# Kernel optimization log

Hardware: AMD Instinct MI355X
Metric: run time of the kernel (lower is better)

Reference implementation:

```python
import jax, jax.numpy as jnp
import numpy as np

NPOINT = 1024   # samples (farthest point sampling count)
RADIUS = 0.2    # ball query radius
K = 32          # neighbors per ball


def farthest_point_sample(xyz, npoint):
    # xyz: [B, N, 3] -> idx: [B, npoint] int32
    B, N, _ = xyz.shape
    def body(carry, _):
        dists, farthest = carry                      # [B,N], [B]
        centroid = jnp.take_along_axis(xyz, farthest[:, None, None], axis=1)  # [B,1,3]
        d = jnp.sum((xyz - centroid) ** 2, axis=-1)  # [B,N]
        dists = jnp.minimum(dists, d)
        nxt = jnp.argmax(dists, axis=-1).astype(jnp.int32)
        return (dists, nxt), farthest
    init = (jnp.full((B, N), 1e10, dtype=xyz.dtype), jnp.zeros((B,), jnp.int32))
    _, idx = jax.lax.scan(body, init, None, length=npoint)
    return jnp.transpose(idx)  # [B, npoint]


def query_ball_point(radius, k, xyz, new_xyz):
    # returns idx: [B, S, k] int32 -- first k in-radius point indices,
    # padded with the first found index (TF query_ball_point semantics)
    N = xyz.shape[1]
    sqd = jnp.sum((new_xyz[:, :, None, :] - xyz[:, None, :, :]) ** 2, axis=-1)  # [B,S,N]
    cand = jnp.where(sqd <= radius * radius, jnp.arange(N, dtype=jnp.int32)[None, None, :], N)
    idx = jnp.sort(cand, axis=-1)[..., :k]          # [B,S,k]
    first = idx[..., :1]
    return jnp.where(idx == N, first, idx).astype(jnp.int32)


def group_point(x, idx):
    # x: [B,N,C], idx: [B,S,k] -> [B,S,k,C]
    return jax.vmap(lambda xb, ib: xb[ib])(x, idx)


def setup_inputs() -> dict:
    key = jax.random.key(0)
    ks = jax.random.split(key, 8)
    B, N, C = 16, 4096, 64
    xyz = jax.random.uniform(ks[0], (B, N, 3), dtype=jnp.float32)
    points = jax.random.normal(ks[1], (B, N, C), dtype=jnp.float32)
    cin = 3 + C  # use_xyz concat
    widths = [64, 64, 128]
    W, b, c = [], [], cin
    for i, w in enumerate(widths):
        W.append(jax.random.normal(ks[2 + i], (c, w), dtype=jnp.float32) * (1.0 / np.sqrt(c)))
        b.append(jnp.zeros((w,), dtype=jnp.float32))
        c = w
    return {"xyz": xyz, "points": points,
            "W0": W[0], "b0": b[0], "W1": W[1], "b1": b[1], "W2": W[2], "b2": b[2]}


def reference(xyz, points, W0, b0, W1, b1, W2, b2):
    # --- sample_and_group ---
    fps_idx = farthest_point_sample(xyz, NPOINT)                 # [B,S]
    new_xyz = jax.vmap(lambda xb, ib: xb[ib])(xyz, fps_idx)      # [B,S,3]
    idx = query_ball_point(RADIUS, K, xyz, new_xyz)              # [B,S,K]
    grouped_xyz = group_point(xyz, idx) - new_xyz[:, :, None, :] # [B,S,K,3]
    grouped_points = group_point(points, idx)                    # [B,S,K,C]
    new_points = jnp.concatenate([grouped_xyz, grouped_points], axis=-1)  # [B,S,K,3+C]
    # --- shared 1x1-conv MLP (bn=False, relu) ---
    for W, bb in ((W0, b0), (W1, b1), (W2, b2)):
        new_points = jax.nn.relu(jnp.einsum('bskc,cd->bskd', new_points, W) + bb)
    # --- max pool over neighborhood ---
    new_points = jnp.max(new_points, axis=2)                     # [B,S,Cout]
    return new_xyz, new_points, idx
```

## Files before the change

### kernel.cpp

```cpp
#include <hip/hip_runtime.h>

#define BB 16
#define NN 4096
#define SS 1024
#define KNB 32
#define FPT 16
#define FNW 4

typedef unsigned long long ull;

__device__ __forceinline__ float sqd3(float dx, float dy, float dz) {
    return __fadd_rn(__fadd_rn(__fmul_rn(dx, dx), __fmul_rn(dy, dy)), __fmul_rn(dz, dz));
}

#define DPPMAX(m, ctrl, rm)                                                              \
    {                                                                                    \
        unsigned _t = (unsigned)__builtin_amdgcn_update_dpp((int)(m), (int)(m), (ctrl),  \
                                                            (rm), 0xf, false);           \
        (m) = ((m) > _t) ? (m) : _t;                                                     \
    }

__global__ __launch_bounds__(256) void fused1_kernel(const float* __restrict__ xyz,
                                                     const float* __restrict__ points,
                                                     const float* __restrict__ W0,
                                                     const float* __restrict__ b0,
                                                     float* __restrict__ P1,
                                                     float* __restrict__ out_newxyz) {
    __shared__ union {
        struct {
            float4 pts[NN];
            ull    keys[2][FNW];
            int    hist[SS];
        } f;
        float w0s[67 * 64];
    } sm;

    const int t = threadIdx.x;

    if (blockIdx.x < BB) {
        const int b = blockIdx.x;
        const int lane = t & 63;
        const float* src = xyz + (size_t)b * (NN * 3) + (size_t)t * (FPT * 3);

        float px[FPT], py[FPT], pz[FPT], dist[FPT];
        {
            float c48[48];
#pragma unroll
            for (int m = 0; m < 12; ++m) {
                float4 v = ((const float4*)src)[m];
                c48[4 * m + 0] = v.x; c48[4 * m + 1] = v.y;
                c48[4 * m + 2] = v.z; c48[4 * m + 3] = v.w;
            }
#pragma unroll
            for (int j = 0; j < FPT; ++j) {
                px[j] = c48[3 * j + 0];
                py[j] = c48[3 * j + 1];
                pz[j] = c48[3 * j + 2];
                dist[j] = 1e10f;
                sm.f.pts[t * FPT + j] = make_float4(px[j], py[j], pz[j], 0.f);
            }
        }
        __syncthreads();

        int far = 0;
        for (int it = 0; it < SS; ++it) {
            if (t == 0) sm.f.hist[it] = far;
            if (it == SS - 1) break;
            float4 c = sm.f.pts[far];

            float bv = -1.f;
            int bn = 0;
#pragma unroll
            for (int j = 0; j < FPT; ++j) {
                float d = sqd3(px[j] - c.x, py[j] - c.y, pz[j] - c.z);
                float dj = fminf(dist[j], d);
                dist[j] = dj;
                bool g = dj > bv;
                bv = g ? dj : bv;
                bn = g ? (t * FPT + j) : bn;
            }

            unsigned mb = __float_as_uint(bv);
            DPPMAX(mb, 0x111, 0xf);
            DPPMAX(mb, 0x112, 0xf);
            DPPMAX(mb, 0x114, 0xf);
            DPPMAX(mb, 0x118, 0xf);
            DPPMAX(mb, 0x142, 0xa);
            DPPMAX(mb, 0x143, 0xc);
            unsigned vmb = (unsigned)__builtin_amdgcn_readlane((int)mb, 63);

            ull ball = __ballot(__float_as_uint(bv) == vmb);
            int sel = __ffsll(ball) - 1;
            int widx = __builtin_amdgcn_readlane(bn, sel);

            const int par = it & 1;
            if (lane == 0) {
                const int wv = t >> 6;
                sm.f.keys[par][wv] = ((ull)vmb << 32) | (unsigned)(~widx);
            }
            __syncthreads();
            const ull* kp = &sm.f.keys[par][0];
            ull k0 = kp[0], k1 = kp[1], k2 = kp[2], k3 = kp[3];
            ull a0 = (k0 > k1) ? k0 : k1;
            ull a1 = (k2 > k3) ? k2 : k3;
            ull best = (a0 > a1) ? a0 : a1;
            far = (int)(~(unsigned)best);
        }
        __syncthreads();
#pragma unroll
        for (int r = 0; r < 4; ++r) {
            int it2 = t + 256 * r;
            int fi = sm.f.hist[it2];
            float4 c = sm.f.pts[fi];
            size_t o = ((size_t)b * SS + it2) * 3;
            out_newxyz[o + 0] = c.x;
            out_newxyz[o + 1] = c.y;
            out_newxyz[o + 2] = c.z;
        }
    } else {
        for (int i = t; i < 67 * 64; i += 256) sm.w0s[i] = W0[i];
        __syncthreads();
        const int lane = t & 63;
        const int wv = t >> 6;
        const float bias = b0[lane];
        const int base = (blockIdx.x - BB) * 256 + wv * 64;
        for (int pi = 0; pi < 64; ++pi) {
            const int n = base + pi;
            const float* xp = xyz + (size_t)n * 3;
            const float* pp = points + (size_t)n * 64;
            float acc = bias;
            acc = fmaf(xp[0], sm.w0s[0 * 64 + lane], acc);
            acc = fmaf(xp[1], sm.w0s[1 * 64 + lane], acc);
            acc = fmaf(xp[2], sm.w0s[2 * 64 + lane], acc);
#pragma unroll 8
            for (int c = 0; c < 64; ++c) acc = fmaf(pp[c], sm.w0s[(3 + c) * 64 + lane], acc);
            P1[(size_t)n * 64 + lane] = acc;
        }
    }
}

__global__ __launch_bounds__(256) void k3_kernel(const float* __restrict__ xyz,
                                                 const float* __restrict__ P1,
                                                 const float* __restrict__ W0,
                                                 const float* __restrict__ W1,
                                                 const float* __restrict__ b1,
                                                 const float* __restrict__ W2,
                                                 const float* __restrict__ b2,
                                                 float* __restrict__ d_out) {
    const int t = threadIdx.x;
    const int lane = t & 63;
    const int wv = t >> 6;
    const int b = blockIdx.x >> 10;

    __shared__ int   ids[KNB];
    __shared__ int   s_cnt;
    __shared__ float part[4][128];
    __shared__ float h1s[4][8][64];
    __shared__ float h2s[4][8][64];

    float* out_newxyz = d_out;
    float* out_points = d_out + (size_t)BB * SS * 3;
    float* out_idx    = d_out + (size_t)BB * SS * 3 + (size_t)BB * SS * 128;

    const size_t q = (size_t)blockIdx.x;
    const float nx = out_newxyz[q * 3 + 0];
    const float ny = out_newxyz[q * 3 + 1];
    const float nz = out_newxyz[q * 3 + 2];

    if (wv == 0) {
        const float* xb = xyz + (size_t)b * (NN * 3);
        const float R2 = 0.04f;
        const ull ltmask = (1ull << lane) - 1ull;
        int total = 0;
        for (int c0 = 0; c0 < NN && total < KNB; c0 += 128) {
            const float* xp0 = xb + (size_t)(c0 + lane) * 3;
            const float* xp1 = xb + (size_t)(c0 + 64 + lane) * 3;
            float d0 = sqd3(xp0[0] - nx, xp0[1] - ny, xp0[2] - nz);
            float d1 = sqd3(xp1[0] - nx, xp1[1] - ny, xp1[2] - nz);
            bool in0 = (d0 <= R2);
            bool in1 = (d1 <= R2);
            ull m0 = __ballot(in0);
            ull m1 = __ballot(in1);
            int pc0 = __popcll(m0);
            int pos0 = total + __popcll(m0 & ltmask);
            int pos1 = total + pc0 + __popcll(m1 & ltmask);
            if (in0 && pos0 < KNB) ids[pos0] = c0 + lane;
            if (in1 && pos1 < KNB) ids[pos1] = c0 + 64 + lane;
            total += pc0 + __popcll(m1);
        }
        if (lane == 0) s_cnt = (total < KNB) ? total : KNB;
    }

    const float qv = nx * W0[lane] + ny * W0[64 + lane] + nz * W0[128 + lane];

    float w1col[64];
#pragma unroll
    for (int i = 0; i < 64; ++i) w1col[i] = W1[i * 64 + lane];
    const float b1v = b1[lane];

    __syncthreads();
    const int cnt = s_cnt;
    if (t >= cnt && t < KNB) ids[t] = ids[0];
    __syncthreads();
    if (t < KNB) out_idx[q * KNB + t] = (float)ids[t];

    const float* P1b = P1 + (size_t)b * NN * 64;
#pragma unroll
    for (int kk = 0; kk < 8; ++kk) {
        int n = ids[wv * 8 + kk];
        float v = P1b[(size_t)n * 64 + lane] - qv;
        h1s[wv][kk][lane] = fmaxf(v, 0.f);
    }

    float acc[8];
#pragma unroll
    for (int kk = 0; kk < 8; ++kk) acc[kk] = b1v;
#pragma unroll
    for (int qd = 0; qd < 16; ++qd) {
#pragma unroll
        for (int kk = 0; kk < 8; ++kk) {
            float4 h4 = *(const float4*)&h1s[wv][kk][4 * qd];
            acc[kk] = fmaf(h4.x, w1col[4 * qd + 0], acc[kk]);
            acc[kk] = fmaf(h4.y, w1col[4 * qd + 1], acc[kk]);
            acc[kk] = fmaf(h4.z, w1col[4 * qd + 2], acc[kk]);
            acc[kk] = fmaf(h4.w, w1col[4 * qd + 3], acc[kk]);
        }
    }
#pragma unroll
    for (int kk = 0; kk < 8; ++kk) h2s[wv][kk][lane] = fmaxf(acc[kk], 0.f);

    float outmax[2];
#pragma unroll
    for (int p = 0; p < 2; ++p) {
        float w2col[64];
#pragma unroll
        for (int i = 0; i < 64; ++i) w2col[i] = W2[i * 128 + 64 * p + lane];
        const float b2v = b2[64 * p + lane];
        float acc3[8];
#pragma unroll
        for (int kk = 0; kk < 8; ++kk) acc3[kk] = b2v;
#pragma unroll
        for (int qd = 0; qd < 16; ++qd) {
#pragma unroll
            for (int kk = 0; kk < 8; ++kk) {
                float4 h4 = *(const float4*)&h2s[wv][kk][4 * qd];
                acc3[kk] = fmaf(h4.x, w2col[4 * qd + 0], acc3[kk]);
                acc3[kk] = fmaf(h4.y, w2col[4 * qd + 1], acc3[kk]);
                acc3[kk] = fmaf(h4.z, w2col[4 * qd + 2], acc3[kk]);
                acc3[kk] = fmaf(h4.w, w2col[4 * qd + 3], acc3[kk]);
            }
        }
        float m = 0.f;
#pragma unroll
        for (int kk = 0; kk < 8; ++kk) m = fmaxf(m, acc3[kk]);
        outmax[p] = m;
    }
    part[wv][lane] = outmax[0];
    part[wv][64 + lane] = outmax[1];
    __syncthreads();
    if (t < 128) {
        float v = fmaxf(fmaxf(part[0][t], part[1][t]), fmaxf(part[2][t], part[3][t]));
        out_points[q * 128 + t] = v;
    }
}

extern "C" void kernel_launch(void* const* d_in, const int* in_sizes, int n_in,
                              void* d_out, int out_size, void* d_ws, size_t ws_size,
                              hipStream_t stream) {
    const float* xyz    = (const float*)d_in[0];
    const float* points = (const float*)d_in[1];
    const float* W0     = (const float*)d_in[2];
    const float* b0     = (const float*)d_in[3];
    const float* W1     = (const float*)d_in[4];
    const float* b1     = (const float*)d_in[5];
    const float* W2     = (const float*)d_in[6];
    const float* b2     = (const float*)d_in[7];
    float* out = (float*)d_out;
    float* P1  = (float*)d_ws;

    hipLaunchKernelGGL(fused1_kernel, dim3(BB + (BB * NN) / 256), dim3(256), 0, stream,
                       xyz, points, W0, b0, P1, out);
    hipLaunchKernelGGL(k3_kernel, dim3(BB * SS), dim3(256), 0, stream,
                       xyz, P1, W0, W1, b1, W2, b2, out);
}
```

Baseline: 773.1 us.

## Packed-math FPS with centroid broadcast and block-wide ball query over float4 xyz

The farthest point sampling loop now uses two-wide float vectors for the distance update. Each wave's winner writes its centroid coordinates alongside its key, so the next iteration no longer has to do a dependent shared-memory load of pts[far]. The ball query now uses all four waves over 256 points per step on a padded float4 copy of xyz written by the P1 blocks, with prefetching. The cost is one extra block barrier per chunk. The changes target the serial FPS critical path and the single-wave ball-query latency.

After: 863.6 us. 1.12x slower.

```diff
diff --git a/kernel.cpp b/kernel.cpp
--- a/kernel.cpp
+++ b/kernel.cpp
@@ -8,6 +8,7 @@
 #define FNW 4
 
 typedef unsigned long long ull;
+typedef float v2f __attribute__((ext_vector_type(2)));
 
 __device__ __forceinline__ float sqd3(float dx, float dy, float dz) {
     return __fadd_rn(__fadd_rn(__fmul_rn(dx, dx), __fmul_rn(dy, dy)), __fmul_rn(dz, dz));
@@ -25,11 +26,15 @@
                                                      const float* __restrict__ W0,
                                                      const float* __restrict__ b0,
                                                      float* __restrict__ P1,
+                                                     float4* __restrict__ xyz4,
                                                      float* __restrict__ out_newxyz) {
     __shared__ union {
         struct {
-            float4 pts[NN];
-            ull    keys[2][FNW];
+            float4 pts4[NN];
+            ull    rkey[2][FNW];
+            float  rx[2][FNW];
+            float  ry[2][FNW];
+            float  rz[2][FNW];
             int    hist[SS];
         } f;
         float w0s[67 * 64];
@@ -40,9 +45,10 @@
     if (blockIdx.x < BB) {
         const int b = blockIdx.x;
         const int lane = t & 63;
+        const int wv = t >> 6;
         const float* src = xyz + (size_t)b * (NN * 3) + (size_t)t * (FPT * 3);
 
-        float px[FPT], py[FPT], pz[FPT], dist[FPT];
+        v2f px2[8], py2[8], pz2[8], d2[8];
         {
             float c48[48];
 #pragma unroll
@@ -52,32 +58,45 @@
                 c48[4 * m + 2] = v.z; c48[4 * m + 3] = v.w;
             }
 #pragma unroll
-            for (int j = 0; j < FPT; ++j) {
-                px[j] = c48[3 * j + 0];
-                py[j] = c48[3 * j + 1];
-                pz[j] = c48[3 * j + 2];
-                dist[j] = 1e10f;
-                sm.f.pts[t * FPT + j] = make_float4(px[j], py[j], pz[j], 0.f);
+            for (int j = 0; j < 8; ++j) {
+                px2[j] = (v2f){c48[6 * j + 0], c48[6 * j + 3]};
+                py2[j] = (v2f){c48[6 * j + 1], c48[6 * j + 4]};
+                pz2[j] = (v2f){c48[6 * j + 2], c48[6 * j + 5]};
+                d2[j]  = (v2f){1e10f, 1e10f};
+                sm.f.pts4[t * FPT + 2 * j + 0] = make_float4(px2[j].x, py2[j].x, pz2[j].x, 0.f);
+                sm.f.pts4[t * FPT + 2 * j + 1] = make_float4(px2[j].y, py2[j].y, pz2[j].y, 0.f);
             }
         }
         __syncthreads();
 
+        float4 cv = sm.f.pts4[0];
+        float cx = cv.x, cy = cv.y, cz = cv.z;
         int far = 0;
         for (int it = 0; it < SS; ++it) {
             if (t == 0) sm.f.hist[it] = far;
             if (it == SS - 1) break;
-            float4 c = sm.f.pts[far];
 
             float bv = -1.f;
             int bn = 0;
-#pragma unroll
-            for (int j = 0; j < FPT; ++j) {
-                float d = sqd3(px[j] - c.x, py[j] - c.y, pz[j] - c.z);
-                float dj = fminf(dist[j], d);
-                dist[j] = dj;
-                bool g = dj > bv;
-                bv = g ? dj : bv;
-                bn = g ? (t * FPT + j) : bn;
+            {
+#pragma clang fp contract(off)
+                v2f cx2 = {cx, cx}, cy2 = {cy, cy}, cz2 = {cz, cz};
+#pragma unroll
+                for (int j = 0; j < 8; ++j) {
+                    v2f dx = px2[j] - cx2;
+                    v2f dy = py2[j] - cy2;
+                    v2f dz = pz2[j] - cz2;
+                    v2f s = (dx * dx + dy * dy) + dz * dz;
+                    float d0 = fminf(d2[j].x, s.x);
+                    float d1 = fminf(d2[j].y, s.y);
+                    d2[j] = (v2f){d0, d1};
+                    bool g0 = d0 > bv;
+                    bv = g0 ? d0 : bv;
+                    bn = g0 ? (t * FPT + 2 * j + 0) : bn;
+                    bool g1 = d1 > bv;
+                    bv = g1 ? d1 : bv;
+                    bn = g1 ? (t * FPT + 2 * j + 1) : bn;
+                }
             }
 
             unsigned mb = __float_as_uint(bv);
@@ -91,27 +110,38 @@
 
             ull ball = __ballot(__float_as_uint(bv) == vmb);
             int sel = __ffsll(ball) - 1;
-            int widx = __builtin_amdgcn_readlane(bn, sel);
-
+            int bnw = __builtin_amdgcn_readlane(bn, sel);
+
+            float4 wc = sm.f.pts4[bnw];
             const int par = it & 1;
-            if (lane == 0) {
-                const int wv = t >> 6;
-                sm.f.keys[par][wv] = ((ull)vmb << 32) | (unsigned)(~widx);
+            if (lane == sel) {
+                sm.f.rkey[par][wv] = ((ull)vmb << 32) | (unsigned)(~bnw);
+                sm.f.rx[par][wv] = wc.x;
+                sm.f.ry[par][wv] = wc.y;
+                sm.f.rz[par][wv] = wc.z;
             }
             __syncthreads();
-            const ull* kp = &sm.f.keys[par][0];
-            ull k0 = kp[0], k1 = kp[1], k2 = kp[2], k3 = kp[3];
-            ull a0 = (k0 > k1) ? k0 : k1;
-            ull a1 = (k2 > k3) ? k2 : k3;
-            ull best = (a0 > a1) ? a0 : a1;
-            far = (int)(~(unsigned)best);
+
+            ull k0 = sm.f.rkey[par][0], k1 = sm.f.rkey[par][1];
+            ull k2 = sm.f.rkey[par][2], k3 = sm.f.rkey[par][3];
+            float x0 = sm.f.rx[par][0], x1 = sm.f.rx[par][1], x2 = sm.f.rx[par][2], x3 = sm.f.rx[par][3];
+            float y0 = sm.f.ry[par][0], y1 = sm.f.ry[par][1], y2 = sm.f.ry[par][2], y3 = sm.f.ry[par][3];
+            float z0 = sm.f.rz[par][0], z1 = sm.f.rz[par][1], z2 = sm.f.rz[par][2], z3 = sm.f.rz[par][3];
+            bool ga = k1 > k0;
+            ull ka = ga ? k1 : k0; float xa = ga ? x1 : x0; float ya = ga ? y1 : y0; float za = ga ? z1 : z0;
+            bool gb = k3 > k2;
+            ull kb = gb ? k3 : k2; float xb = gb ? x3 : x2; float yb = gb ? y3 : y2; float zb = gb ? z3 : z2;
+            bool gc = kb > ka;
+            ull kf = gc ? kb : ka;
+            cx = gc ? xb : xa; cy = gc ? yb : ya; cz = gc ? zb : za;
+            far = (int)(~(unsigned)kf);
         }
         __syncthreads();
 #pragma unroll
         for (int r = 0; r < 4; ++r) {
             int it2 = t + 256 * r;
             int fi = sm.f.hist[it2];
-            float4 c = sm.f.pts[fi];
+            float4 c = sm.f.pts4[fi];
             size_t o = ((size_t)b * SS + it2) * 3;
             out_newxyz[o + 0] = c.x;
             out_newxyz[o + 1] = c.y;
@@ -122,6 +152,12 @@
         __syncthreads();
         const int lane = t & 63;
         const int wv = t >> 6;
+
+        {
+            int n0 = (blockIdx.x - BB) * 256 + t;
+            xyz4[n0] = make_float4(xyz[3 * n0 + 0], xyz[3 * n0 + 1], xyz[3 * n0 + 2], 0.f);
+        }
+
         const float bias = b0[lane];
         const int base = (blockIdx.x - BB) * 256 + wv * 64;
         for (int pi = 0; pi < 64; ++pi) {
@@ -139,7 +175,7 @@
     }
 }
 
-__global__ __launch_bounds__(256) void k3_kernel(const float* __restrict__ xyz,
+__global__ __launch_bounds__(256) void k3_kernel(const float4* __restrict__ xyz4,
                                                  const float* __restrict__ P1,
                                                  const float* __restrict__ W0,
                                                  const float* __restrict__ W1,
@@ -153,10 +189,9 @@
     const int b = blockIdx.x >> 10;
 
     __shared__ int   ids[KNB];
-    __shared__ int   s_cnt;
+    __shared__ int   bq[2][FNW];
     __shared__ float part[4][128];
-    __shared__ float h1s[4][8][64];
-    __shared__ float h2s[4][8][64];
+    __shared__ float hs[4][8][64];
 
     float* out_newxyz = d_out;
     float* out_points = d_out + (size_t)BB * SS * 3;
@@ -167,40 +202,40 @@
     const float ny = out_newxyz[q * 3 + 1];
     const float nz = out_newxyz[q * 3 + 2];
 
-    if (wv == 0) {
-        const float* xb = xyz + (size_t)b * (NN * 3);
-        const float R2 = 0.04f;
-        const ull ltmask = (1ull << lane) - 1ull;
-        int total = 0;
-        for (int c0 = 0; c0 < NN && total < KNB; c0 += 128) {
-            const float* xp0 = xb + (size_t)(c0 + lane) * 3;
-            const float* xp1 = xb + (size_t)(c0 + 64 + lane) * 3;
-            float d0 = sqd3(xp0[0] - nx, xp0[1] - ny, xp0[2] - nz);
-            float d1 = sqd3(xp1[0] - nx, xp1[1] - ny, xp1[2] - nz);
-            bool in0 = (d0 <= R2);
-            bool in1 = (d1 <= R2);
-            ull m0 = __ballot(in0);
-            ull m1 = __ballot(in1);
-            int pc0 = __popcll(m0);
-            int pos0 = total + __popcll(m0 & ltmask);
-            int pos1 = total + pc0 + __popcll(m1 & ltmask);
-            if (in0 && pos0 < KNB) ids[pos0] = c0 + lane;
-            if (in1 && pos1 < KNB) ids[pos1] = c0 + 64 + lane;
-            total += pc0 + __popcll(m1);
-        }
-        if (lane == 0) s_cnt = (total < KNB) ? total : KNB;
-    }
-
     const float qv = nx * W0[lane] + ny * W0[64 + lane] + nz * W0[128 + lane];
-
     float w1col[64];
 #pragma unroll
     for (int i = 0; i < 64; ++i) w1col[i] = W1[i * 64 + lane];
     const float b1v = b1[lane];
 
-    __syncthreads();
-    const int cnt = s_cnt;
-    if (t >= cnt && t < KNB) ids[t] = ids[0];
+    {
+        const float4* xb4 = xyz4 + (size_t)b * NN;
+        const float R2 = 0.04f;
+        const ull ltm = (1ull << lane) - 1ull;
+        int total = 0, c0 = 0, pr = 0;
+        float4 pc = xb4[t];
+        while (true) {
+            float4 cur = pc;
+            int nc0 = c0 + 256;
+            if (nc0 < NN) pc = xb4[nc0 + t];
+            float d = sqd3(cur.x - nx, cur.y - ny, cur.z - nz);
+            bool in = (d <= R2);
+            ull m = __ballot(in);
+            if (lane == 0) bq[pr][wv] = __popcll(m);
+            __syncthreads();
+            int q0 = bq[pr][0], q1 = bq[pr][1], q2 = bq[pr][2], q3 = bq[pr][3];
+            int basew = total + (wv > 0 ? q0 : 0) + (wv > 1 ? q1 : 0) + (wv > 2 ? q2 : 0);
+            int pos = basew + __popcll(m & ltm);
+            if (in && pos < KNB) ids[pos] = c0 + t;
+            total += q0 + q1 + q2 + q3;
+            c0 = nc0;
+            pr ^= 1;
+            if (total >= KNB || c0 >= NN) break;
+        }
+        __syncthreads();
+        int cnt = (total < KNB) ? total : KNB;
+        if (t >= cnt && t < KNB) ids[t] = ids[0];
+    }
     __syncthreads();
     if (t < KNB) out_idx[q * KNB + t] = (float)ids[t];
 
@@ -209,7 +244,7 @@
     for (int kk = 0; kk < 8; ++kk) {
         int n = ids[wv * 8 + kk];
         float v = P1b[(size_t)n * 64 + lane] - qv;
-        h1s[wv][kk][lane] = fmaxf(v, 0.f);
+        hs[wv][kk][lane] = fmaxf(v, 0.f);
     }
 
     float acc[8];
@@ -219,7 +254,7 @@
     for (int qd = 0; qd < 16; ++qd) {
 #pragma unroll
         for (int kk = 0; kk < 8; ++kk) {
-            float4 h4 = *(const float4*)&h1s[wv][kk][4 * qd];
+            float4 h4 = *(const float4*)&hs[wv][kk][4 * qd];
             acc[kk] = fmaf(h4.x, w1col[4 * qd + 0], acc[kk]);
             acc[kk] = fmaf(h4.y, w1col[4 * qd + 1], acc[kk]);
             acc[kk] = fmaf(h4.z, w1col[4 * qd + 2], acc[kk]);
@@ -227,7 +262,7 @@
         }
     }
 #pragma unroll
-    for (int kk = 0; kk < 8; ++kk) h2s[wv][kk][lane] = fmaxf(acc[kk], 0.f);
+    for (int kk = 0; kk < 8; ++kk) hs[wv][kk][lane] = fmaxf(acc[kk], 0.f);
 
     float outmax[2];
 #pragma unroll
@@ -243,7 +278,7 @@
         for (int qd = 0; qd < 16; ++qd) {
 #pragma unroll
             for (int kk = 0; kk < 8; ++kk) {
-                float4 h4 = *(const float4*)&h2s[wv][kk][4 * qd];
+                float4 h4 = *(const float4*)&hs[wv][kk][4 * qd];
                 acc3[kk] = fmaf(h4.x, w2col[4 * qd + 0], acc3[kk]);
                 acc3[kk] = fmaf(h4.y, w2col[4 * qd + 1], acc3[kk]);
                 acc3[kk] = fmaf(h4.z, w2col[4 * qd + 2], acc3[kk]);
@@ -276,10 +311,11 @@
     const float* W2     = (const float*)d_in[6];
     const float* b2     = (const float*)d_in[7];
     float* out = (float*)d_out;
-    float* P1  = (float*)d_ws;
+    float*  P1   = (float*)d_ws;
+    float4* xyz4 = (float4*)((char*)d_ws + (size_t)BB * NN * 64 * 4);
 
     hipLaunchKernelGGL(fused1_kernel, dim3(BB + (BB * NN) / 256), dim3(256), 0, stream,
-                       xyz, points, W0, b0, P1, out);
+                       xyz, points, W0, b0, P1, xyz4, out);
     hipLaunchKernelGGL(k3_kernel, dim3(BB * SS), dim3(256), 0, stream,
-                       xyz, P1, W0, W1, b1, W2, b2, out);
+                       xyz4, P1, W0, W1, b1, W2, b2, out);
 }
```
